# Optimization experiments

Hardware: AMD Instinct MI355X
Metric: run time of the kernel (lower is better)

The kernel has to match this reference:

```python
import jax, jax.numpy as jnp
import numpy as np
from jax.scipy.special import logsumexp

B, F, V, C, K, KP = 8192, 32, 64, 32, 8, 7  # batch, features, values/feature, classes, gate options, padded pair candidates
TEMP = 1.0
EPS = 1e-06


def _structure():
    # candidate 0 = self table; candidates 1..7 = pair tables conditioned on preceding features
    mask = np.zeros((F - 1, K), dtype=bool)
    mask[:, 0] = True
    cond = np.zeros((F - 1, KP), dtype=np.int32)
    for i in range(F - 1):
        fi = i + 1
        for j in range(min(fi, KP)):
            mask[i, j + 1] = True
            cond[i, j] = fi - 1 - j
    return jnp.asarray(cond), jnp.asarray(mask)


def setup_inputs() -> dict:
    key = jax.random.key(0)
    ks = jax.random.split(key, 6)
    cond_index, valid_mask = _structure()
    return {
        "x": jax.random.randint(ks[0], (B, F), 0, V, dtype=jnp.int32),
        "training": True,
        "class_logits": jax.random.normal(ks[1], (C,), jnp.float32) * 0.1,
        "table0": jax.random.normal(ks[2], (V, C), jnp.float32) * 0.1,
        "self_tables": jax.random.normal(ks[3], (F - 1, V, C), jnp.float32) * 0.1,
        "pair_tables": jax.random.normal(ks[4], (F - 1, KP, V, V, C), jnp.float32) * 0.1,
        "structure_logits": jax.random.normal(ks[5], (F - 1, K), jnp.float32) * 0.1,
        "u_noise": jax.random.uniform(jax.random.fold_in(key, 7), (F - 1, K), jnp.float32),
        "cond_index": cond_index,
        "valid_mask": valid_mask,
    }


def reference(x, training, class_logits, table0, self_tables, pair_tables,
              structure_logits, u_noise, cond_index, valid_mask):
    # class prior term
    cl = class_logits - logsumexp(class_logits)  # [C]
    t0 = table0 - logsumexp(table0, axis=0, keepdims=True)  # [V,C]
    out = cl[None, :] + t0[x[:, 0]]  # [B,C]

    # Gumbel-softmax gate over candidate parent sets (training path)
    g = -jnp.log(-jnp.log(u_noise + EPS) + EPS)
    gate_logits = jnp.where(valid_mask, (structure_logits + g) / TEMP, -jnp.inf)
    w = jax.nn.softmax(gate_logits, axis=-1)  # [F-1,K]; padded entries get weight 0

    f_idx = jnp.arange(F - 1)
    xs = x[:, 1:]  # [B,F-1] feature values

    # self (class-only) candidate tables, normalized over the feature-value axis
    st = self_tables - logsumexp(self_tables, axis=1, keepdims=True)  # [F-1,V,C]
    self_g = st[f_idx[None, :], xs]  # [B,F-1,C]
    out = out + jnp.einsum('bfc,f->bc', self_g, w[:, 0])

    # pair candidate tables, normalized over the feature-value axis (axis 2)
    pt = pair_tables - logsumexp(pair_tables, axis=2, keepdims=True)  # [F-1,KP,V,V,C]
    xc = x[:, cond_index]  # [B,F-1,KP] conditioning feature values
    k_idx = jnp.arange(KP)
    pair_g = pt[f_idx[None, :, None], k_idx[None, None, :], xs[:, :, None], xc]  # [B,F-1,KP,C]
    out = out + jnp.einsum('bfkc,fk->bc', pair_g, w[:, 1:])
    return out
```

## Files before the change

kernel.cpp:

```cpp
#include <hip/hip_runtime.h>
#include <math.h>

#define B_  8192
#define F_  32
#define V_  64
#define C_  32
#define KP_ 7
#define EPS_ 1e-6f

#define WS_OFF  256
#define WS_G    512
#define WS_LSE  66048
#define LSE_BANK4 111104
#define WS_PART 1843712

#define NBLK_LSE 868
#define NBLK_PAIR 2048

__device__ const int d_split[9] = {0, 25, 50, 74, 99, 123, 148, 172, 196};

__global__ __launch_bounds__(256)
void fused_kernel(const int* __restrict__ x, const float* __restrict__ pt,
                  const float* __restrict__ cl, const float* __restrict__ t0,
                  const float* __restrict__ st, const float* __restrict__ sl,
                  const float* __restrict__ un, float* __restrict__ ws) {
    if (blockIdx.x < NBLK_LSE) {
        int fk = blockIdx.x >> 2;
        int qa = blockIdx.x & 3;
        int t  = threadIdx.x;
        const float4* __restrict__ p =
            (const float4*)(pt + (size_t)fk * (V_ * V_ * C_)
                               + (size_t)qa * 16 * (V_ * C_));
        const float4* p0 = p + t;
        const float4* p1 = p + 256 + t;
        float4 s0 = make_float4(0.f, 0.f, 0.f, 0.f);
        float4 s1 = make_float4(0.f, 0.f, 0.f, 0.f);
        #pragma unroll 4
        for (int a = 0; a < 16; a++) {
            float4 l0 = p0[a * 512];
            float4 l1 = p1[a * 512];
            s0.x += __expf(l0.x); s0.y += __expf(l0.y);
            s0.z += __expf(l0.z); s0.w += __expf(l0.w);
            s1.x += __expf(l1.x); s1.y += __expf(l1.y);
            s1.z += __expf(l1.z); s1.w += __expf(l1.w);
        }
        float4* lseP = (float4*)(ws + WS_LSE) + (size_t)qa * LSE_BANK4;
        lseP[fk * 512 + t]       = s0;
        lseP[fk * 512 + 256 + t] = s1;
    } else if (blockIdx.x == NBLK_LSE) {
        __shared__ float gl[31][8];
        __shared__ float wsm[31][8];
        __shared__ float lsf[31][32];
        int tid = threadIdx.x;
        if (tid < 248) {
            int f = tid >> 3, k = tid & 7;
            int kmax = min(f + 1, KP_);
            bool valid = (k <= kmax);
            float u = un[tid];
            float g = -__logf(-__logf(u + EPS_) + EPS_);
            gl[f][k] = valid ? (sl[tid] + g) : -INFINITY;
        } else {
            ws[tid] = 0.f;
        }
        __syncthreads();
        if (tid < 248) {
            int f = tid >> 3, k = tid & 7;
            float m = -INFINITY;
            #pragma unroll
            for (int j = 0; j < 8; j++) m = fmaxf(m, gl[f][j]);
            float s = 0.f;
            #pragma unroll
            for (int j = 0; j < 8; j++) s += __expf(gl[f][j] - m);
            float wv = __expf(gl[f][k] - m) / s;
            wsm[f][k] = wv;
            ws[tid] = wv;
        }
        for (int i = tid; i < 992; i += 256) {
            int f = i >> 5, c = i & 31;
            float s = 0.f;
            #pragma unroll 8
            for (int v = 0; v < V_; v++) s += __expf(st[(f * V_ + v) * C_ + c]);
            lsf[f][c] = __logf(s);
        }
        __syncthreads();
        if (tid < 32) {
            int c = tid;
            float scl = 0.f;
            #pragma unroll
            for (int j = 0; j < C_; j++) scl += __expf(cl[j]);
            float lse_cl = __logf(scl);
            float s0 = 0.f;
            #pragma unroll 8
            for (int v = 0; v < V_; v++) s0 += __expf(t0[v * C_ + c]);
            float lse_t0 = __logf(s0);
            float acc = cl[c] - lse_cl - lse_t0;
            for (int f = 0; f < 31; f++) acc -= wsm[f][0] * lsf[f][c];
            ws[WS_OFF + c] = acc;
        }
    } else {
        __shared__ int    xsh[4 * 33];
        __shared__ float  wsh[256];
        __shared__ int    etab[200];
        __shared__ float4 part[7][32];
        __shared__ float  gl[31][8];
        int tid = threadIdx.x;
        int pb  = blockIdx.x - (NBLK_LSE + 1);
        if (tid < 128) xsh[(tid >> 5) * 33 + (tid & 31)] = x[pb * 128 + tid];
        if (tid < 248) {
            int f = tid >> 3, k = tid & 7;
            int kmax = min(f + 1, KP_);
            bool valid = (k <= kmax);
            float u = un[tid];
            float g = -__logf(-__logf(u + EPS_) + EPS_);
            gl[f][k] = valid ? (sl[tid] + g) : -INFINITY;
        }
        if (tid < 200) {
            int q = tid / 25, i = tid % 25;
            int g = d_split[q] + i;
            int packed;
            if (g < d_split[q + 1]) {
                int f = 0, base = 0;
                for (;;) { int cnt = min(f + 1, KP_); if (g < base + cnt) break; base += cnt; f++; }
                int k = g - base;
                packed = ((f * 8 + k + 1) << 20) | ((f * KP_ + k) << 12) | ((f + 1) << 6) | (f - k);
            } else {
                packed = (248 << 20);
            }
            etab[tid] = packed;
        }
        __syncthreads();
        if (tid < 248) {
            int f = tid >> 3;
            float m = -INFINITY;
            #pragma unroll
            for (int j = 0; j < 8; j++) m = fmaxf(m, gl[f][j]);
            float s = 0.f;
            #pragma unroll
            for (int j = 0; j < 8; j++) s += __expf(gl[f][j] - m);
            wsh[tid] = __expf(gl[f][tid & 7] - m) / s;
        } else {
            wsh[tid] = 0.f;
        }
        __syncthreads();

        int q  = tid >> 5;
        int r  = (tid >> 3) & 3;
        int c4 = tid & 7;
        const int* xrow = &xsh[r * 33];
        const float* __restrict__ ptb = pt + c4 * 4;
        float4 acc = make_float4(0.f, 0.f, 0.f, 0.f);

        int beg = q * 25;
        #pragma unroll
        for (int ch = 0; ch < 5; ch++) {
            float4 pv[5];
            float  wt[5];
            #pragma unroll
            for (int i = 0; i < 5; i++) {
                int pk = etab[beg + ch * 5 + i];
                int ci = pk & 63, fi = (pk >> 6) & 63;
                int fk = (pk >> 12) & 255, widx = (pk >> 20) & 255;
                int xv = xrow[fi], xc = xrow[ci];
                pv[i] = *(const float4*)(ptb + ((size_t)(fk * V_ + xv) * V_ + xc) * C_);
                wt[i] = wsh[widx];
            }
            #pragma unroll
            for (int i = 0; i < 5; i++) {
                acc.x += wt[i] * pv[i].x; acc.y += wt[i] * pv[i].y;
                acc.z += wt[i] * pv[i].z; acc.w += wt[i] * pv[i].w;
            }
        }

        if (q > 0) part[q - 1][r * 8 + c4] = acc;
        __syncthreads();
        if (q == 0) {
            #pragma unroll
            for (int p = 0; p < 7; p++) {
                float4 pv2 = part[p][r * 8 + c4];
                acc.x += pv2.x; acc.y += pv2.y; acc.z += pv2.z; acc.w += pv2.w;
            }
            ((float4*)(ws + WS_PART))[(pb * 4 + r) * 8 + c4] = acc;
        }
    }
}

__global__ __launch_bounds__(256)
void foldg_kernel(const float* __restrict__ t0, const float* __restrict__ st,
                  float* __restrict__ ws) {
    int idx = blockIdx.x * 256 + threadIdx.x;
    int c4 = idx & 7, v = (idx >> 3) & 63, j = idx >> 9;
    int nk = min(KP_, 31 - j);
    const float4* lse4 = (const float4*)(ws + WS_LSE);
    float4 g;
    if (j == 0) {
        g = ((const float4*)t0)[v * 8 + c4];
    } else {
        float w0 = ws[(j - 1) * 8];
        float4 sv = ((const float4*)st)[((j - 1) * V_ + v) * 8 + c4];
        g.x = w0 * sv.x; g.y = w0 * sv.y; g.z = w0 * sv.z; g.w = w0 * sv.w;
    }
    for (int k = 0; k < nk; k++) {
        int f = j + k;
        float wv = ws[f * 8 + k + 1];
        int iq = ((f * KP_ + k) * V_ + v) * 8 + c4;
        float4 sa = lse4[iq];
        float4 sb = lse4[1 * LSE_BANK4 + iq];
        float4 sc = lse4[2 * LSE_BANK4 + iq];
        float4 sd = lse4[3 * LSE_BANK4 + iq];
        g.x -= wv * __logf(sa.x + sb.x + sc.x + sd.x);
        g.y -= wv * __logf(sa.y + sb.y + sc.y + sd.y);
        g.z -= wv * __logf(sa.z + sb.z + sc.z + sd.z);
        g.w -= wv * __logf(sa.w + sb.w + sc.w + sd.w);
    }
    ((float4*)(ws + WS_G))[idx] = g;
}

__global__ __launch_bounds__(256)
void maing_kernel(const int* __restrict__ x, const float* __restrict__ ws,
                  float* __restrict__ out) {
    __shared__ int    xsh[32][33];
    __shared__ float4 offv[8];
    int tid = threadIdx.x;
    int rbase = blockIdx.x * 32;
    for (int i = tid; i < 1024; i += 256) {
        int rr = i >> 5, jj = i & 31;
        xsh[rr][jj] = x[(rbase + rr) * 32 + jj];
    }
    if (tid < 8) offv[tid] = ((const float4*)(ws + WS_OFF))[tid];
    __syncthreads();
    int r = tid >> 3, c4 = tid & 7;
    const float4* __restrict__ G4 = (const float4*)(ws + WS_G);
    float4 acc = ((const float4*)(ws + WS_PART))[(rbase + r) * 8 + c4];
    float4 ov = offv[c4];
    acc.x += ov.x; acc.y += ov.y; acc.z += ov.z; acc.w += ov.w;
    #pragma unroll 8
    for (int j = 0; j < 32; j++) {
        float4 gv = G4[(j * V_ + xsh[r][j]) * 8 + c4];
        acc.x += gv.x; acc.y += gv.y; acc.z += gv.z; acc.w += gv.w;
    }
    ((float4*)out)[(rbase + r) * 8 + c4] = acc;
}

extern "C" void kernel_launch(void* const* d_in, const int* in_sizes, int n_in,
                              void* d_out, int out_size, void* d_ws, size_t ws_size,
                              hipStream_t stream) {
    const int*   x   = (const int*)  d_in[0];
    const float* cl  = (const float*)d_in[2];
    const float* t0  = (const float*)d_in[3];
    const float* st  = (const float*)d_in[4];
    const float* pt  = (const float*)d_in[5];
    const float* sl  = (const float*)d_in[6];
    const float* un  = (const float*)d_in[7];
    float* ws  = (float*)d_ws;
    float* out = (float*)d_out;

    fused_kernel<<<NBLK_LSE + 1 + NBLK_PAIR, 256, 0, stream>>>(x, pt, cl, t0, st, sl, un, ws);
    foldg_kernel<<<64, 256, 0, stream>>>(t0, st, ws);
    maing_kernel<<<256, 256, 0, stream>>>(x, ws, out);
}
```

Before: 223.7 us.

## Split LSE from pair gather; fuse fold into pair kernel with per-group partials

```diff
diff --git a/kernel.cpp b/kernel.cpp
--- a/kernel.cpp
+++ b/kernel.cpp
@@ -16,14 +16,15 @@
 
 #define NBLK_LSE 868
 #define NBLK_PAIR 2048
+#define NBLK_FOLD 64
 
 __device__ const int d_split[9] = {0, 25, 50, 74, 99, 123, 148, 172, 196};
 
 __global__ __launch_bounds__(256)
-void fused_kernel(const int* __restrict__ x, const float* __restrict__ pt,
-                  const float* __restrict__ cl, const float* __restrict__ t0,
-                  const float* __restrict__ st, const float* __restrict__ sl,
-                  const float* __restrict__ un, float* __restrict__ ws) {
+void lse_prep_kernel(const float* __restrict__ pt,
+                     const float* __restrict__ cl, const float* __restrict__ t0,
+                     const float* __restrict__ st, const float* __restrict__ sl,
+                     const float* __restrict__ un, float* __restrict__ ws) {
     if (blockIdx.x < NBLK_LSE) {
         int fk = blockIdx.x >> 2;
         int qa = blockIdx.x & 3;
@@ -47,7 +48,7 @@
         float4* lseP = (float4*)(ws + WS_LSE) + (size_t)qa * LSE_BANK4;
         lseP[fk * 512 + t]       = s0;
         lseP[fk * 512 + 256 + t] = s1;
-    } else if (blockIdx.x == NBLK_LSE) {
+    } else {
         __shared__ float gl[31][8];
         __shared__ float wsm[31][8];
         __shared__ float lsf[31][32];
@@ -97,31 +98,41 @@
             for (int f = 0; f < 31; f++) acc -= wsm[f][0] * lsf[f][c];
             ws[WS_OFF + c] = acc;
         }
-    } else {
-        __shared__ int    xsh[4 * 33];
-        __shared__ float  wsh[256];
-        __shared__ int    etab[200];
-        __shared__ float4 part[7][32];
-        __shared__ float  gl[31][8];
+    }
+}
+
+__global__ __launch_bounds__(256)
+void pair_fold_kernel(const int* __restrict__ x, const float* __restrict__ pt,
+                      const float* __restrict__ t0, const float* __restrict__ st,
+                      const float* __restrict__ sl, const float* __restrict__ un,
+                      float* __restrict__ ws) {
+    if (blockIdx.x < NBLK_PAIR) {
+        __shared__ int   xsh[32][33];
+        __shared__ float wsh[256];
+        __shared__ int   etab[200];
+        __shared__ float gl[31][8];
         int tid = threadIdx.x;
-        int pb  = blockIdx.x - (NBLK_LSE + 1);
-        if (tid < 128) xsh[(tid >> 5) * 33 + (tid & 31)] = x[pb * 128 + tid];
+        int g     = blockIdx.x & 7;
+        int chunk = blockIdx.x >> 3;
+        int s0    = chunk * 32;
+        for (int i = tid; i < 1024; i += 256)
+            xsh[i >> 5][i & 31] = x[s0 * 32 + i];
         if (tid < 248) {
             int f = tid >> 3, k = tid & 7;
             int kmax = min(f + 1, KP_);
             bool valid = (k <= kmax);
             float u = un[tid];
-            float g = -__logf(-__logf(u + EPS_) + EPS_);
-            gl[f][k] = valid ? (sl[tid] + g) : -INFINITY;
+            float gg = -__logf(-__logf(u + EPS_) + EPS_);
+            gl[f][k] = valid ? (sl[tid] + gg) : -INFINITY;
         }
         if (tid < 200) {
             int q = tid / 25, i = tid % 25;
-            int g = d_split[q] + i;
+            int e = d_split[q] + i;
             int packed;
-            if (g < d_split[q + 1]) {
+            if (e < d_split[q + 1]) {
                 int f = 0, base = 0;
-                for (;;) { int cnt = min(f + 1, KP_); if (g < base + cnt) break; base += cnt; f++; }
-                int k = g - base;
+                for (;;) { int cnt = min(f + 1, KP_); if (e < base + cnt) break; base += cnt; f++; }
+                int k = e - base;
                 packed = ((f * 8 + k + 1) << 20) | ((f * KP_ + k) << 12) | ((f + 1) << 6) | (f - k);
             } else {
                 packed = (248 << 20);
@@ -143,14 +154,13 @@
         }
         __syncthreads();
 
-        int q  = tid >> 5;
-        int r  = (tid >> 3) & 3;
+        int s  = tid >> 3;
         int c4 = tid & 7;
-        const int* xrow = &xsh[r * 33];
+        const int* xrow = xsh[s];
         const float* __restrict__ ptb = pt + c4 * 4;
         float4 acc = make_float4(0.f, 0.f, 0.f, 0.f);
 
-        int beg = q * 25;
+        int beg = g * 25;
         #pragma unroll
         for (int ch = 0; ch < 5; ch++) {
             float4 pv[5];
@@ -170,49 +180,35 @@
                 acc.z += wt[i] * pv[i].z; acc.w += wt[i] * pv[i].w;
             }
         }
-
-        if (q > 0) part[q - 1][r * 8 + c4] = acc;
-        __syncthreads();
-        if (q == 0) {
-            #pragma unroll
-            for (int p = 0; p < 7; p++) {
-                float4 pv2 = part[p][r * 8 + c4];
-                acc.x += pv2.x; acc.y += pv2.y; acc.z += pv2.z; acc.w += pv2.w;
-            }
-            ((float4*)(ws + WS_PART))[(pb * 4 + r) * 8 + c4] = acc;
-        }
-    }
-}
-
-__global__ __launch_bounds__(256)
-void foldg_kernel(const float* __restrict__ t0, const float* __restrict__ st,
-                  float* __restrict__ ws) {
-    int idx = blockIdx.x * 256 + threadIdx.x;
-    int c4 = idx & 7, v = (idx >> 3) & 63, j = idx >> 9;
-    int nk = min(KP_, 31 - j);
-    const float4* lse4 = (const float4*)(ws + WS_LSE);
-    float4 g;
-    if (j == 0) {
-        g = ((const float4*)t0)[v * 8 + c4];
+        ((float4*)(ws + WS_PART))[(size_t)(s0 + s) * 64 + g * 8 + c4] = acc;
     } else {
-        float w0 = ws[(j - 1) * 8];
-        float4 sv = ((const float4*)st)[((j - 1) * V_ + v) * 8 + c4];
-        g.x = w0 * sv.x; g.y = w0 * sv.y; g.z = w0 * sv.z; g.w = w0 * sv.w;
-    }
-    for (int k = 0; k < nk; k++) {
-        int f = j + k;
-        float wv = ws[f * 8 + k + 1];
-        int iq = ((f * KP_ + k) * V_ + v) * 8 + c4;
-        float4 sa = lse4[iq];
-        float4 sb = lse4[1 * LSE_BANK4 + iq];
-        float4 sc = lse4[2 * LSE_BANK4 + iq];
-        float4 sd = lse4[3 * LSE_BANK4 + iq];
-        g.x -= wv * __logf(sa.x + sb.x + sc.x + sd.x);
-        g.y -= wv * __logf(sa.y + sb.y + sc.y + sd.y);
-        g.z -= wv * __logf(sa.z + sb.z + sc.z + sd.z);
-        g.w -= wv * __logf(sa.w + sb.w + sc.w + sd.w);
-    }
-    ((float4*)(ws + WS_G))[idx] = g;
+        int idx = (blockIdx.x - NBLK_PAIR) * 256 + threadIdx.x;
+        int c4 = idx & 7, v = (idx >> 3) & 63, j = idx >> 9;
+        int nk = min(KP_, 31 - j);
+        const float4* lse4 = (const float4*)(ws + WS_LSE);
+        float4 gv;
+        if (j == 0) {
+            gv = ((const float4*)t0)[v * 8 + c4];
+        } else {
+            float w0 = ws[(j - 1) * 8];
+            float4 sv = ((const float4*)st)[((j - 1) * V_ + v) * 8 + c4];
+            gv.x = w0 * sv.x; gv.y = w0 * sv.y; gv.z = w0 * sv.z; gv.w = w0 * sv.w;
+        }
+        for (int k = 0; k < nk; k++) {
+            int f = j + k;
+            float wv = ws[f * 8 + k + 1];
+            int iq = ((f * KP_ + k) * V_ + v) * 8 + c4;
+            float4 sa = lse4[iq];
+            float4 sb = lse4[1 * LSE_BANK4 + iq];
+            float4 sc = lse4[2 * LSE_BANK4 + iq];
+            float4 sd = lse4[3 * LSE_BANK4 + iq];
+            gv.x -= wv * __logf(sa.x + sb.x + sc.x + sd.x);
+            gv.y -= wv * __logf(sa.y + sb.y + sc.y + sd.y);
+            gv.z -= wv * __logf(sa.z + sb.z + sc.z + sd.z);
+            gv.w -= wv * __logf(sa.w + sb.w + sc.w + sd.w);
+        }
+        ((float4*)(ws + WS_G))[idx] = gv;
+    }
 }
 
 __global__ __launch_bounds__(256)
@@ -230,9 +226,14 @@
     __syncthreads();
     int r = tid >> 3, c4 = tid & 7;
     const float4* __restrict__ G4 = (const float4*)(ws + WS_G);
-    float4 acc = ((const float4*)(ws + WS_PART))[(rbase + r) * 8 + c4];
-    float4 ov = offv[c4];
-    acc.x += ov.x; acc.y += ov.y; acc.z += ov.z; acc.w += ov.w;
+    float4 acc = offv[c4];
+    const float4* __restrict__ pp =
+        (const float4*)(ws + WS_PART) + (size_t)(rbase + r) * 64 + c4;
+    #pragma unroll
+    for (int g = 0; g < 8; g++) {
+        float4 t = pp[g * 8];
+        acc.x += t.x; acc.y += t.y; acc.z += t.z; acc.w += t.w;
+    }
     #pragma unroll 8
     for (int j = 0; j < 32; j++) {
         float4 gv = G4[(j * V_ + xsh[r][j]) * 8 + c4];
@@ -254,7 +255,7 @@
     float* ws  = (float*)d_ws;
     float* out = (float*)d_out;
 
-    fused_kernel<<<NBLK_LSE + 1 + NBLK_PAIR, 256, 0, stream>>>(x, pt, cl, t0, st, sl, un, ws);
-    foldg_kernel<<<64, 256, 0, stream>>>(t0, st, ws);
+    lse_prep_kernel<<<NBLK_LSE + 1, 256, 0, stream>>>(pt, cl, t0, st, sl, un, ws);
+    pair_fold_kernel<<<NBLK_PAIR + NBLK_FOLD, 256, 0, stream>>>(x, pt, t0, st, sl, un, ws);
     maing_kernel<<<256, 256, 0, stream>>>(x, ws, out);
 }
```

After: 231.1 us. 1.03x slower.
